# Optimization experiments

Hardware: AMD Instinct MI355X
Metric: run time of the kernel (lower is better)

The kernel has to match this reference:

```python
import jax, jax.numpy as jnp
import numpy as np

D, NH, DH, L, NCP, TW, NTP = 256, 8, 32, 4, 4, 2, 2
P = NCP + TW * NTP  # points per level per head
SHAPES = np.array([[4, 48, 64], [4, 24, 32], [4, 12, 16], [4, 6, 8]], dtype=np.int64)  # (T, H, W) per level


def _offset_biases():
    # Faithful to _reset_parameters: directional grid init for sampling-offset biases.
    thetas = np.arange(NH, dtype=np.float64) * (2.0 * np.pi / NH)
    grid = np.stack([np.cos(thetas), np.sin(thetas)], -1)
    grid = grid / np.abs(grid).max(-1, keepdims=True)
    curr = np.tile(grid.reshape(NH, 1, 1, 2), (1, L, NCP, 1))
    for i in range(NCP):
        curr[:, :, i, :] *= i + 1
    temp = np.tile(grid.reshape(NH, 1, 1, 1, 2), (1, L, TW, NTP, 1))
    init_offset = 0
    for pos, t in enumerate(range(1, TW + 1)):  # encoder default branch
        if t % 2:
            init_offset += 1
        for i in range(NTP):
            temp[:, :, pos, i, :] *= i + 1 + init_offset
    return curr.reshape(-1).astype(np.float32), temp.reshape(-1).astype(np.float32)


def setup_inputs() -> dict:
    key = jax.random.key(0)
    k = jax.random.split(key, 10)
    sizes = SHAPES[:, 0] * SHAPES[:, 1] * SHAPES[:, 2]
    Len_in = int(sizes.sum())  # 16320
    Lq, N = Len_in, 1
    b_so_np, b_tso_np = _offset_biases()
    return {
        "query": jax.random.normal(k[0], (N, Lq, D), jnp.float32),
        "reference_points": jax.random.uniform(k[1], (N, Lq, L, 2), jnp.float32),
        "temporal_offsets": jax.random.normal(k[2], (Lq, L, TW, 2), jnp.float32) * 0.02,
        "input_flatten": jax.random.normal(k[3], (N, Len_in, D), jnp.float32),
        "input_spatial_shapes": jnp.asarray(SHAPES),
        "input_level_start_index": jnp.asarray(np.concatenate([[0], np.cumsum(sizes)[:-1]]).astype(np.int64)),
        "W_so": jax.random.normal(k[4], (D, NH * L * NCP * 2), jnp.float32) * 0.01,
        "b_so": jnp.asarray(b_so_np),
        "W_tso": jax.random.normal(k[5], (D, NH * L * TW * NTP * 2), jnp.float32) * 0.01,
        "b_tso": jnp.asarray(b_tso_np),
        "W_aw": jax.random.normal(k[6], (D, NH * L * NCP), jnp.float32) * 0.02,
        "b_aw": jnp.zeros((NH * L * NCP,), jnp.float32),
        "W_taw": jax.random.normal(k[7], (D, NH * L * TW * NTP), jnp.float32) * 0.02,
        "b_taw": jnp.zeros((NH * L * TW * NTP,), jnp.float32),
        "W_v": jax.random.normal(k[8], (D, D), jnp.float32) / np.sqrt(D),
        "b_v": jnp.zeros((D,), jnp.float32),
        "W_o": jax.random.normal(k[9], (D, D), jnp.float32) / np.sqrt(D),
        "b_o": jnp.zeros((D,), jnp.float32),
    }


def _deform_core(value, loc, attn):
    # value: (N, Len_in, NH, DH); loc: (N, Lq, NH, L, P, 2) in [0,1]; attn: (N, Lq, NH, L, P)
    N, Lq = loc.shape[0], loc.shape[1]
    out = jnp.zeros((N, NH, Lq, DH), value.dtype)
    start = 0
    for l in range(L):  # small fixed level loop
        t, h, w = (int(s) for s in SHAPES[l])
        th = t * h  # frames stacked vertically -> grid is (T*H, W)
        npix = th * w
        v = value[:, start:start + npix].transpose(0, 2, 1, 3)  # (N, NH, npix, DH)
        # grid_sample semantics, align_corners=False, zero padding
        x = loc[:, :, :, l, :, 0] * w - 0.5
        y = loc[:, :, :, l, :, 1] * th - 0.5
        x0 = jnp.floor(x); y0 = jnp.floor(y)
        lx = x - x0; ly = y - y0
        x0i = x0.astype(jnp.int32); y0i = y0.astype(jnp.int32)

        def corner(xi, yi, wgt):
            inb = (xi >= 0) & (xi < w) & (yi >= 0) & (yi < th)
            idx = jnp.clip(yi, 0, th - 1) * w + jnp.clip(xi, 0, w - 1)  # (N,Lq,NH,P)
            idx = idx.transpose(0, 2, 1, 3).reshape(N, NH, Lq * P, 1)
            g = jnp.take_along_axis(v, idx, axis=2).reshape(N, NH, Lq, P, DH)
            wm = (wgt * inb).transpose(0, 2, 1, 3)  # (N,NH,Lq,P)
            return g * wm[..., None]

        samp = (corner(x0i, y0i, (1 - lx) * (1 - ly))
                + corner(x0i + 1, y0i, lx * (1 - ly))
                + corner(x0i, y0i + 1, (1 - lx) * ly)
                + corner(x0i + 1, y0i + 1, lx * ly))
        a = attn[:, :, :, l].transpose(0, 2, 1, 3)  # (N,NH,Lq,P)
        out = out + (samp * a[..., None]).sum(3)
        start += npix
    return out.transpose(0, 2, 1, 3).reshape(N, Lq, D)


def _forward(query, reference_points, temporal_offsets, input_flatten,
             W_so, b_so, W_tso, b_tso, W_aw, b_aw, W_taw, b_taw, W_v, b_v, W_o, b_o):
    N, Lq, _ = query.shape
    value = (input_flatten @ W_v + b_v).reshape(N, -1, NH, DH)
    cso = (query @ W_so + b_so).reshape(N, Lq, NH, L, NCP, 2)
    tso = (query @ W_tso + b_tso).reshape(N, Lq, NH, L, TW, NTP, 2)
    caw = (query @ W_aw + b_aw).reshape(N, Lq, NH, L * NCP)
    taw = (query @ W_taw + b_taw).reshape(N, Lq, NH, L * TW * NTP)
    aw = jax.nn.softmax(jnp.concatenate([caw, taw], -1), -1)  # joint softmax over curr+temporal
    attn = jnp.concatenate([aw[..., :L * NCP].reshape(N, Lq, NH, L, NCP),
                            aw[..., L * NCP:].reshape(N, Lq, NH, L, TW * NTP)], -1)
    # offset_normalizer = [W, T*H] per level
    norm = jnp.asarray(np.stack([SHAPES[:, 2], SHAPES[:, 0] * SHAPES[:, 1]], -1).astype(np.float32))
    tso_n = temporal_offsets[None, :, None, :, :, None, :] + tso / norm[None, None, None, :, None, None, :]
    tso_n = tso_n.reshape(N, Lq, NH, L, TW * NTP, 2)
    cso_n = cso / norm[None, None, None, :, None, :]
    loc = reference_points[:, :, None, :, None, :] + jnp.concatenate([cso_n, tso_n], 4)  # (N,Lq,NH,L,P,2)
    out = _deform_core(value, loc, attn)
    return out @ W_o + b_o


def reference(query, reference_points, temporal_offsets, input_flatten,
              input_spatial_shapes, input_level_start_index,
              W_so, b_so, W_tso, b_tso, W_aw, b_aw, W_taw, b_taw, W_v, b_v, W_o, b_o):
    return _forward(query, reference_points, temporal_offsets, input_flatten,
                    W_so, b_so, W_tso, b_tso, W_aw, b_aw, W_taw, b_taw, W_v, b_v, W_o, b_o)
```

## Files before the change

### kernel.cpp

```cpp
#include <hip/hip_runtime.h>


typedef unsigned short bfraw;
typedef __attribute__((ext_vector_type(2))) float f32x2;
typedef __attribute__((ext_vector_type(4))) float f32x4;
typedef __attribute__((ext_vector_type(8))) short bf16x8;

__device__ __forceinline__ float bf2f(bfraw u) {
  union { unsigned int i; float f; } v; v.i = ((unsigned int)u) << 16; return v.f;
}
__device__ __forceinline__ bfraw f2bf(float f) {
  union { float f; unsigned int i; } v; v.f = f;
  unsigned int x = v.i;
  return (bfraw)((x + 0x7FFFu + ((x >> 16) & 1u)) >> 16);
}
__device__ __forceinline__ float lo16f(unsigned int w) {
  union { unsigned int i; float f; } v; v.i = w << 16; return v.f;
}
__device__ __forceinline__ float hi16f(unsigned int w) {
  union { unsigned int i; float f; } v; v.i = w & 0xFFFF0000u; return v.f;
}
__device__ __forceinline__ float loadx(const void* p, size_t i, int f32m) {
  if (f32m) return ((const float*)p)[i];
  else      return bf2f(((const bfraw*)p)[i]);
}
__device__ __forceinline__ unsigned pk2(float a, float b) {
  return (unsigned)f2bf(a) | ((unsigned)f2bf(b) << 16);
}

__device__ __forceinline__ int vote_f32(const void* q) {
  const unsigned* p = (const unsigned*)q;
  int cnt = 0;
#pragma unroll
  for (int i = 0; i < 16; ++i) {
    const float a = fabsf(lo16f(p[i]));
    cnt += (a > 0.0009765625f && a < 16.0f) ? 1 : 0;
  }
  return (cnt >= 8) ? 0 : 1;
}

__device__ __forceinline__ void cvt8(const void* src, bfraw* dst, int i0, int f32m) {
  if (f32m) {
    const float4 a = ((const float4*)((const float*)src + i0))[0];
    const float4 b = ((const float4*)((const float*)src + i0))[1];
    uint4 o;
    o.x = pk2(a.x, a.y); o.y = pk2(a.z, a.w);
    o.z = pk2(b.x, b.y); o.w = pk2(b.z, b.w);
    *(uint4*)(dst + i0) = o;
  } else {
    *(uint4*)(dst + i0) = *(const uint4*)((const bfraw*)src + i0);
  }
}

__global__ __launch_bounds__(256) void prep_k(
    const void* W_v, const void* W_so, const void* W_tso,
    const void* W_aw, const void* W_taw, const void* W_o,
    const void* b_so, const void* b_tso, const void* b_aw, const void* b_taw,
    const void* b_v, const void* b_o,
    const void* refp, const void* toff,
    const void* query, const void* inflat,
    bfraw* __restrict__ WT, float* __restrict__ bcat,
    float* __restrict__ refpF, float* __restrict__ toffF,
    bfraw* __restrict__ queryB, bfraw* __restrict__ inflatB,
    int qbf, int ibf)
{
  const int f32m = vote_f32(query);
  const int b = blockIdx.x, t = threadIdx.x;
  if (b < 1280) {
    float s;
    if (b < 256)       s = loadx(W_v, (size_t)t * 256 + b, f32m);
    else if (b < 1024) {
      const int rp = b - 256;
      if (rp < 256)      s = loadx(W_so,  (size_t)t * 256 + rp, f32m);
      else if (rp < 512) s = loadx(W_tso, (size_t)t * 256 + (rp - 256), f32m);
      else if (rp < 640) s = loadx(W_aw,  (size_t)t * 128 + (rp - 512), f32m);
      else               s = loadx(W_taw, (size_t)t * 128 + (rp - 640), f32m);
    } else               s = loadx(W_o,  (size_t)t * 256 + (b - 1024), f32m);
    WT[(size_t)b * 256 + t] = f2bf(s);
  } else if (b < 1285) {
    const int i = (b - 1280) * 256 + t;
    if (i < 1280) {
      float s;
      if (i < 256)       s = loadx(b_so,  i, f32m);
      else if (i < 512)  s = loadx(b_tso, i - 256, f32m);
      else if (i < 640)  s = loadx(b_aw,  i - 512, f32m);
      else if (i < 768)  s = loadx(b_taw, i - 640, f32m);
      else if (i < 1024) s = loadx(b_v,   i - 768, f32m);
      else               s = loadx(b_o,   i - 1024, f32m);
      bcat[i] = s;
    }
  } else if (b < 1795) {
    const int i = (b - 1285) * 256 + t;
    refpF[i] = loadx(refp, i, f32m);
  } else if (b < 2815) {
    const int i = (b - 1795) * 256 + t;
    toffF[i] = loadx(toff, i, f32m);
  } else if (b < 4855) {
    if (!qbf) return;
    cvt8(query, queryB, (b - 2815) * 2048 + t * 8, f32m);
  } else {
    if (!ibf) return;
    cvt8(inflat, inflatB, (b - 4855) * 2048 + t * 8, f32m);
  }
}

__global__ __launch_bounds__(256) void gemmVP_k(
    const void* __restrict__ inflat, const void* __restrict__ query,
    const bfraw* __restrict__ inflatB, const bfraw* __restrict__ queryB,
    const bfraw* __restrict__ WT, const float* __restrict__ bcat,
    bfraw* __restrict__ valueOut, bfraw* __restrict__ proj, int M,
    int ibf, int qbf)
{
  __shared__ bfraw As[128][40];
  __shared__ bfraw Bs[128][40];
  const int y = blockIdx.y;
  const void* Araw; const bfraw* Abf; int wtb, colb, bmode, abf;
  if (y < 2) { Araw = inflat; Abf = inflatB; abf = ibf;
               wtb = y * 128;             colb = y * 128;       bmode = 1; }
  else       { Araw = query;  Abf = queryB;  abf = qbf;
               wtb = 256 + (y - 2) * 128; colb = (y - 2) * 128; bmode = 0; }
  const int f32m = abf ? 0 : vote_f32(query);

  const int bm = blockIdx.x * 128;
  const int tid = threadIdx.x;
  const int wave = tid >> 6, lane = tid & 63;
  const int quad = lane >> 4, l16 = lane & 15;
  const int mb = (wave >> 1) * 64, nb = (wave & 1) * 64;
  const int srow = tid >> 1;
  const int sk = (tid & 1) * 16;

  int lr = bm + srow; if (lr >= M) lr = M - 1;
  const size_t aoff = (size_t)lr * 256;

  f32x4 acc[4][4] = {{{0.f}}};

  for (int k0 = 0; k0 < 256; k0 += 32) {
    uint4 pa0, pa1;
    if (abf) {
      const bfraw* Ab = Abf + aoff + (k0 + sk);
      pa0 = ((const uint4*)Ab)[0];
      pa1 = ((const uint4*)Ab)[1];
    } else if (f32m) {
      const float* Af = (const float*)Araw + aoff + (k0 + sk);
      const float4 x0 = ((const float4*)Af)[0];
      const float4 x1 = ((const float4*)Af)[1];
      const float4 x2 = ((const float4*)Af)[2];
      const float4 x3 = ((const float4*)Af)[3];
      pa0.x = pk2(x0.x, x0.y); pa0.y = pk2(x0.z, x0.w);
      pa0.z = pk2(x1.x, x1.y); pa0.w = pk2(x1.z, x1.w);
      pa1.x = pk2(x2.x, x2.y); pa1.y = pk2(x2.z, x2.w);
      pa1.z = pk2(x3.x, x3.y); pa1.w = pk2(x3.z, x3.w);
    } else {
      const bfraw* Ab = (const bfraw*)Araw + aoff + (k0 + sk);
      pa0 = ((const uint4*)Ab)[0];
      pa1 = ((const uint4*)Ab)[1];
    }
    const bfraw* Bb = WT + (size_t)(wtb + srow) * 256 + (k0 + sk);
    const uint4 pb0 = ((const uint4*)Bb)[0];
    const uint4 pb1 = ((const uint4*)Bb)[1];
    *(uint4*)&As[srow][sk]     = pa0;
    *(uint4*)&As[srow][sk + 8] = pa1;
    *(uint4*)&Bs[srow][sk]     = pb0;
    *(uint4*)&Bs[srow][sk + 8] = pb1;
    __syncthreads();

    bf16x8 af[4], bf[4];
#pragma unroll
    for (int i = 0; i < 4; ++i)
      af[i] = *(const bf16x8*)&As[mb + i * 16 + l16][quad * 8];
#pragma unroll
    for (int j = 0; j < 4; ++j)
      bf[j] = *(const bf16x8*)&Bs[nb + j * 16 + l16][quad * 8];
#pragma unroll
    for (int i = 0; i < 4; ++i)
#pragma unroll
      for (int j = 0; j < 4; ++j)
        acc[i][j] = __builtin_amdgcn_mfma_f32_16x16x32_bf16(af[i], bf[j], acc[i][j], 0, 0, 0);
    __syncthreads();
  }

#pragma unroll
  for (int j = 0; j < 4; ++j) {
    const int col = colb + nb + j * 16 + l16;
    const float bb = bmode ? bcat[768 + col] : bcat[col];
#pragma unroll
    for (int i = 0; i < 4; ++i) {
#pragma unroll
      for (int r = 0; r < 4; ++r) {
        const int lrow = bm + mb + i * 16 + quad * 4 + r;
        if (lrow < M) {
          const float vv = acc[i][j][r] + bb;
          if (!bmode)
            proj[(size_t)lrow * 768 + col] = f2bf(vv);
          else
            valueOut[((unsigned)(col >> 5) * (unsigned)M + (unsigned)lrow) * 32u
                     + (unsigned)(col & 31)] = f2bf(vv);
        }
      }
    }
  }
}

__global__ __launch_bounds__(256) void gemmO_k(
    const bfraw* __restrict__ proj, const bfraw* __restrict__ WT,
    const float* __restrict__ bcat, void* __restrict__ Cout,
    const void* __restrict__ query, int M)
{
  __shared__ bfraw As[128][40];
  __shared__ bfraw Bs[128][40];
  const int f32m = vote_f32(query);
  const int bm = blockIdx.x * 128;
  const int bn = blockIdx.y * 128;
  const int tid = threadIdx.x;
  const int wave = tid >> 6, lane = tid & 63;
  const int quad = lane >> 4, l16 = lane & 15;
  const int mb = (wave >> 1) * 64, nb = (wave & 1) * 64;
  const int srow = tid >> 1;
  const int sk = (tid & 1) * 16;

  int lr = bm + srow; if (lr >= M) lr = M - 1;
  const size_t aoff = (size_t)lr * 768;

  f32x4 acc[4][4] = {{{0.f}}};

  for (int k0 = 0; k0 < 256; k0 += 32) {
    const bfraw* Ab = proj + aoff + (k0 + sk);
    const uint4 pa0 = ((const uint4*)Ab)[0];
    const uint4 pa1 = ((const uint4*)Ab)[1];
    const bfraw* Bb = WT + (size_t)(1024 + bn + srow) * 256 + (k0 + sk);
    const uint4 pb0 = ((const uint4*)Bb)[0];
    const uint4 pb1 = ((const uint4*)Bb)[1];
    *(uint4*)&As[srow][sk]     = pa0;
    *(uint4*)&As[srow][sk + 8] = pa1;
    *(uint4*)&Bs[srow][sk]     = pb0;
    *(uint4*)&Bs[srow][sk + 8] = pb1;
    __syncthreads();

    bf16x8 af[4], bf[4];
#pragma unroll
    for (int i = 0; i < 4; ++i)
      af[i] = *(const bf16x8*)&As[mb + i * 16 + l16][quad * 8];
#pragma unroll
    for (int j = 0; j < 4; ++j)
      bf[j] = *(const bf16x8*)&Bs[nb + j * 16 + l16][quad * 8];
#pragma unroll
    for (int i = 0; i < 4; ++i)
#pragma unroll
      for (int j = 0; j < 4; ++j)
        acc[i][j] = __builtin_amdgcn_mfma_f32_16x16x32_bf16(af[i], bf[j], acc[i][j], 0, 0, 0);
    __syncthreads();
  }

#pragma unroll
  for (int j = 0; j < 4; ++j) {
    const int col = bn + nb + j * 16 + l16;
    const float bb = bcat[1024 + col];
#pragma unroll
    for (int i = 0; i < 4; ++i) {
#pragma unroll
      for (int r = 0; r < 4; ++r) {
        const int lrow = bm + mb + i * 16 + quad * 4 + r;
        if (lrow < M) {
          const float v = acc[i][j][r] + bb;
          if (f32m) ((float*)Cout)[(size_t)lrow * 256 + col] = v;
          else      ((bfraw*)Cout)[(size_t)lrow * 256 + col] = f2bf(v);
        }
      }
    }
  }
}

__global__ __launch_bounds__(256) void sampler_k(
    bfraw* __restrict__ proj, const bfraw* __restrict__ value,
    const float* __restrict__ refp, const float* __restrict__ toff)
{
  __shared__ __align__(16) int   s_idx[256][4];
  __shared__ __align__(16) float s_w[256][4];

  const int h = blockIdx.y;
  const int tid = threadIdx.x;
  const int qi = tid >> 5;
  const int sp = tid & 31;
  const int l = sp >> 3;
  const int p = sp & 7;
  const int qg = blockIdx.x * 8 + qi;

  const int W_i[4]  = {64, 32, 16, 8};
  const int TH_i[4] = {192, 96, 48, 24};
  const int ST_i[4] = {0, 12288, 15360, 16128};
  const float Wf  = (float)W_i[l];
  const float THf = (float)TH_i[l];

  bfraw* prow = proj + (size_t)qg * 768;

  const float logit = (p < 4) ? bf2f(prow[512 + h * 16 + l * 4 + p])
                              : bf2f(prow[640 + h * 16 + l * 4 + (p - 4)]);
  float mx = logit;
#pragma unroll
  for (int m = 16; m >= 1; m >>= 1) mx = fmaxf(mx, __shfl_xor(mx, m));
  const float e = __expf(logit - mx);
  float ssum = e;
#pragma unroll
  for (int m = 16; m >= 1; m >>= 1) ssum += __shfl_xor(ssum, m);
  const float attn = e / ssum;

  const float rx = refp[(unsigned)(qg * 4 + l) * 2 + 0];
  const float ry = refp[(unsigned)(qg * 4 + l) * 2 + 1];
  float ox, oy;
  if (p < 4) {
    ox = bf2f(prow[h * 32 + l * 8 + p * 2 + 0]) / Wf;
    oy = bf2f(prow[h * 32 + l * 8 + p * 2 + 1]) / THf;
  } else {
    const int pj = p - 4, tw = pj >> 1, j = pj & 1;
    ox = toff[(unsigned)(qg * 4 + l) * 4 + tw * 2 + 0] +
         bf2f(prow[256 + h * 32 + l * 8 + tw * 4 + j * 2 + 0]) / Wf;
    oy = toff[(unsigned)(qg * 4 + l) * 4 + tw * 2 + 1] +
         bf2f(prow[256 + h * 32 + l * 8 + tw * 4 + j * 2 + 1]) / THf;
  }
  const float x = (rx + ox) * Wf - 0.5f;
  const float y = (ry + oy) * THf - 0.5f;
  const float x0f = floorf(x), y0f = floorf(y);
  const float lx = x - x0f, ly = y - y0f;
  const int x0 = (int)x0f, y0 = (int)y0f;
  const int Wg = W_i[l], THg = TH_i[l], ST = ST_i[l];
  const float cwx[2] = {1.f - lx, lx};
  const float cwy[2] = {1.f - ly, ly};
#pragma unroll
  for (int c = 0; c < 4; ++c) {
    const int xi = x0 + (c & 1), yi = y0 + (c >> 1);
    const bool inb = (xi >= 0) & (xi < Wg) & (yi >= 0) & (yi < THg);
    const int xc = min(max(xi, 0), Wg - 1);
    const int yc = min(max(yi, 0), THg - 1);
    s_idx[tid][c] = ST + yc * Wg + xc;
    s_w[tid][c] = inb ? (attn * cwx[c & 1] * cwy[c >> 1]) : 0.f;
  }
  __syncthreads();

  {
    const int pg = sp >> 2;
    const int chq = sp & 3;
    const char* vb = (const char*)(value + (unsigned)h * (16320u * 32u));
    const unsigned cb = (unsigned)(chq << 4);
    int   idx[16];
    float ww[16];
#pragma unroll
    for (int pt = 0; pt < 4; ++pt) {
      const int ds = qi * 32 + pg * 4 + pt;
      const int4   ia = *(const int4*)&s_idx[ds][0];
      const float4 wa = *(const float4*)&s_w[ds][0];
      idx[pt * 4 + 0] = ia.x; idx[pt * 4 + 1] = ia.y;
      idx[pt * 4 + 2] = ia.z; idx[pt * 4 + 3] = ia.w;
      ww[pt * 4 + 0] = wa.x; ww[pt * 4 + 1] = wa.y;
      ww[pt * 4 + 2] = wa.z; ww[pt * 4 + 3] = wa.w;
    }
#define GLD(n) const uint4 v##n = *(const uint4*)(vb + ((((unsigned)idx[n]) << 6) | cb))
    GLD(0); GLD(1); GLD(2); GLD(3); GLD(4); GLD(5); GLD(6); GLD(7);
    GLD(8); GLD(9); GLD(10); GLD(11); GLD(12); GLD(13); GLD(14); GLD(15);
#undef GLD
    f32x2 a0 = {0.f, 0.f}, a1 = {0.f, 0.f}, a2 = {0.f, 0.f}, a3 = {0.f, 0.f};
#define CONS(n) {                                            \
    const float w = ww[n];                                   \
    const f32x2 w2 = {w, w};                                 \
    f32x2 t;                                                 \
    t.x = lo16f(v##n.x); t.y = hi16f(v##n.x); a0 += w2 * t;  \
    t.x = lo16f(v##n.y); t.y = hi16f(v##n.y); a1 += w2 * t;  \
    t.x = lo16f(v##n.z); t.y = hi16f(v##n.z); a2 += w2 * t;  \
    t.x = lo16f(v##n.w); t.y = hi16f(v##n.w); a3 += w2 * t;  }
    CONS(0); CONS(1); CONS(2); CONS(3); CONS(4); CONS(5); CONS(6); CONS(7);
    CONS(8); CONS(9); CONS(10); CONS(11); CONS(12); CONS(13); CONS(14); CONS(15);
#undef CONS
    float acc[8] = {a0.x, a0.y, a1.x, a1.y, a2.x, a2.y, a3.x, a3.y};
#pragma unroll
    for (int m = 4; m <= 16; m <<= 1)
#pragma unroll
      for (int r = 0; r < 8; ++r)
        acc[r] += __shfl_xor(acc[r], m);
    if (pg == 0) {
      uint4 pk;
      pk.x = pk2(acc[0], acc[1]);
      pk.y = pk2(acc[2], acc[3]);
      pk.z = pk2(acc[4], acc[5]);
      pk.w = pk2(acc[6], acc[7]);
      *(uint4*)(prow + h * 32 + chq * 8) = pk;
    }
  }
}

extern "C" void kernel_launch(void* const* d_in, const int* in_sizes, int n_in,
                              void* d_out, int out_size, void* d_ws, size_t ws_size,
                              hipStream_t stream)
{
  const void* query  = d_in[0];
  const void* refp   = d_in[1];
  const void* toff   = d_in[2];
  const void* inflat = d_in[3];
  const void* W_so  = d_in[6];
  const void* b_so  = d_in[7];
  const void* W_tso = d_in[8];
  const void* b_tso = d_in[9];
  const void* W_aw  = d_in[10];
  const void* b_aw  = d_in[11];
  const void* W_taw = d_in[12];
  const void* b_taw = d_in[13];
  const void* W_v   = d_in[14];
  const void* b_v   = d_in[15];
  const void* W_o   = d_in[16];
  const void* b_o   = d_in[17];

  const int Lq = 16320;
  const size_t WT_B   = (size_t)1280 * 256 * 2;
  const size_t BCAT_B = 1280 * 4;
  const size_t REFP_B = (size_t)Lq * 8 * 4;
  const size_t TOFF_B = (size_t)Lq * 16 * 4;
  const size_t VAL_B  = (size_t)8 * Lq * 32 * 2;
  const size_t PROJ_B = (size_t)Lq * 768 * 2;
  const size_t QB_B   = (size_t)Lq * 256 * 2;
  const size_t base   = WT_B + BCAT_B + REFP_B + TOFF_B + VAL_B + PROJ_B;

  const int qbf = (ws_size >= base + QB_B)     ? 1 : 0;
  const int ibf = (ws_size >= base + 2 * QB_B) ? 1 : 0;

  char* wp = (char*)d_ws;
  bfraw* WT     = (bfraw*)wp; wp += WT_B;
  float* bcat   = (float*)wp; wp += BCAT_B;
  float* refpF  = (float*)wp; wp += REFP_B;
  float* toffF  = (float*)wp; wp += TOFF_B;
  bfraw* value  = (bfraw*)wp; wp += VAL_B;
  bfraw* proj   = (bfraw*)wp; wp += PROJ_B;
  bfraw* queryB = (bfraw*)wp; wp += QB_B;
  bfraw* inflatB= (bfraw*)wp;

  const dim3 blk(256);
  const int prep_blocks = ibf ? 6895 : (qbf ? 4855 : 2815);
  prep_k<<<dim3(prep_blocks), blk, 0, stream>>>(
      W_v, W_so, W_tso, W_aw, W_taw, W_o,
      b_so, b_tso, b_aw, b_taw, b_v, b_o,
      refp, toff, query, inflat,
      WT, bcat, refpF, toffF, queryB, inflatB, qbf, ibf);
  gemmVP_k<<<dim3(128, 8), blk, 0, stream>>>(inflat, query, inflatB, queryB,
                                             WT, bcat, value, proj, Lq, ibf, qbf);
  sampler_k<<<dim3(Lq / 8, 8), blk, 0, stream>>>(proj, value, refpF, toffF);
  gemmO_k<<<dim3(128, 2), blk, 0, stream>>>(proj, WT, bcat, d_out, query, Lq);
}
```

Before: 221.6 us.

## Drop LDS staging in GEMMs and load MFMA fragments directly from global

```diff
diff --git a/kernel.cpp b/kernel.cpp
--- a/kernel.cpp
+++ b/kernel.cpp
@@ -111,8 +111,6 @@
     bfraw* __restrict__ valueOut, bfraw* __restrict__ proj, int M,
     int ibf, int qbf)
 {
-  __shared__ bfraw As[128][40];
-  __shared__ bfraw Bs[128][40];
   const int y = blockIdx.y;
   const void* Araw; const bfraw* Abf; int wtb, colb, bmode, abf;
   if (y < 2) { Araw = inflat; Abf = inflatB; abf = ibf;
@@ -126,59 +124,53 @@
   const int wave = tid >> 6, lane = tid & 63;
   const int quad = lane >> 4, l16 = lane & 15;
   const int mb = (wave >> 1) * 64, nb = (wave & 1) * 64;
-  const int srow = tid >> 1;
-  const int sk = (tid & 1) * 16;
-
-  int lr = bm + srow; if (lr >= M) lr = M - 1;
-  const size_t aoff = (size_t)lr * 256;
+
+  size_t aoff[4]; const bfraw* bptr[4];
+#pragma unroll
+  for (int i = 0; i < 4; ++i) {
+    int row = bm + mb + i * 16 + l16; if (row >= M) row = M - 1;
+    aoff[i] = (size_t)row * 256 + quad * 8;
+  }
+#pragma unroll
+  for (int j = 0; j < 4; ++j)
+    bptr[j] = WT + (size_t)(wtb + nb + j * 16 + l16) * 256 + quad * 8;
 
   f32x4 acc[4][4] = {{{0.f}}};
 
+#pragma unroll
   for (int k0 = 0; k0 < 256; k0 += 32) {
-    uint4 pa0, pa1;
+    bf16x8 af[4], bf[4];
     if (abf) {
-      const bfraw* Ab = Abf + aoff + (k0 + sk);
-      pa0 = ((const uint4*)Ab)[0];
-      pa1 = ((const uint4*)Ab)[1];
+#pragma unroll
+      for (int i = 0; i < 4; ++i)
+        af[i] = *(const bf16x8*)(Abf + aoff[i] + k0);
     } else if (f32m) {
-      const float* Af = (const float*)Araw + aoff + (k0 + sk);
-      const float4 x0 = ((const float4*)Af)[0];
-      const float4 x1 = ((const float4*)Af)[1];
-      const float4 x2 = ((const float4*)Af)[2];
-      const float4 x3 = ((const float4*)Af)[3];
-      pa0.x = pk2(x0.x, x0.y); pa0.y = pk2(x0.z, x0.w);
-      pa0.z = pk2(x1.x, x1.y); pa0.w = pk2(x1.z, x1.w);
-      pa1.x = pk2(x2.x, x2.y); pa1.y = pk2(x2.z, x2.w);
-      pa1.z = pk2(x3.x, x3.y); pa1.w = pk2(x3.z, x3.w);
+#pragma unroll
+      for (int i = 0; i < 4; ++i) {
+        const float* Af = (const float*)Araw + aoff[i] + k0;
+        const float4 x0 = ((const float4*)Af)[0];
+        const float4 x1 = ((const float4*)Af)[1];
+        uint4 o;
+        o.x = pk2(x0.x, x0.y); o.y = pk2(x0.z, x0.w);
+        o.z = pk2(x1.x, x1.y); o.w = pk2(x1.z, x1.w);
+        af[i] = *(const bf16x8*)&o;
+      }
     } else {
-      const bfraw* Ab = (const bfraw*)Araw + aoff + (k0 + sk);
-      pa0 = ((const uint4*)Ab)[0];
-      pa1 = ((const uint4*)Ab)[1];
-    }
-    const bfraw* Bb = WT + (size_t)(wtb + srow) * 256 + (k0 + sk);
-    const uint4 pb0 = ((const uint4*)Bb)[0];
-    const uint4 pb1 = ((const uint4*)Bb)[1];
-    *(uint4*)&As[srow][sk]     = pa0;
-    *(uint4*)&As[srow][sk + 8] = pa1;
-    *(uint4*)&Bs[srow][sk]     = pb0;
-    *(uint4*)&Bs[srow][sk + 8] = pb1;
-    __syncthreads();
-
-    bf16x8 af[4], bf[4];
-#pragma unroll
-    for (int i = 0; i < 4; ++i)
-      af[i] = *(const bf16x8*)&As[mb + i * 16 + l16][quad * 8];
+#pragma unroll
+      for (int i = 0; i < 4; ++i)
+        af[i] = *(const bf16x8*)((const bfraw*)Araw + aoff[i] + k0);
+    }
 #pragma unroll
     for (int j = 0; j < 4; ++j)
-      bf[j] = *(const bf16x8*)&Bs[nb + j * 16 + l16][quad * 8];
+      bf[j] = *(const bf16x8*)(bptr[j] + k0);
 #pragma unroll
     for (int i = 0; i < 4; ++i)
 #pragma unroll
       for (int j = 0; j < 4; ++j)
         acc[i][j] = __builtin_amdgcn_mfma_f32_16x16x32_bf16(af[i], bf[j], acc[i][j], 0, 0, 0);
-    __syncthreads();
-  }
-
+  }
+
+  const int quad4 = quad * 4;
 #pragma unroll
   for (int j = 0; j < 4; ++j) {
     const int col = colb + nb + j * 16 + l16;
@@ -187,7 +179,7 @@
     for (int i = 0; i < 4; ++i) {
 #pragma unroll
       for (int r = 0; r < 4; ++r) {
-        const int lrow = bm + mb + i * 16 + quad * 4 + r;
+        const int lrow = bm + mb + i * 16 + quad4 + r;
         if (lrow < M) {
           const float vv = acc[i][j][r] + bb;
           if (!bmode)
@@ -206,8 +198,6 @@
     const float* __restrict__ bcat, void* __restrict__ Cout,
     const void* __restrict__ query, int M)
 {
-  __shared__ bfraw As[128][40];
-  __shared__ bfraw Bs[128][40];
   const int f32m = vote_f32(query);
   const int bm = blockIdx.x * 128;
   const int bn = blockIdx.y * 128;
@@ -215,42 +205,36 @@
   const int wave = tid >> 6, lane = tid & 63;
   const int quad = lane >> 4, l16 = lane & 15;
   const int mb = (wave >> 1) * 64, nb = (wave & 1) * 64;
-  const int srow = tid >> 1;
-  const int sk = (tid & 1) * 16;
-
-  int lr = bm + srow; if (lr >= M) lr = M - 1;
-  const size_t aoff = (size_t)lr * 768;
+
+  const bfraw* aptr[4]; const bfraw* bptr[4];
+#pragma unroll
+  for (int i = 0; i < 4; ++i) {
+    int row = bm + mb + i * 16 + l16; if (row >= M) row = M - 1;
+    aptr[i] = proj + (size_t)row * 768 + quad * 8;
+  }
+#pragma unroll
+  for (int j = 0; j < 4; ++j)
+    bptr[j] = WT + (size_t)(1024 + bn + nb + j * 16 + l16) * 256 + quad * 8;
 
   f32x4 acc[4][4] = {{{0.f}}};
 
+#pragma unroll
   for (int k0 = 0; k0 < 256; k0 += 32) {
-    const bfraw* Ab = proj + aoff + (k0 + sk);
-    const uint4 pa0 = ((const uint4*)Ab)[0];
-    const uint4 pa1 = ((const uint4*)Ab)[1];
-    const bfraw* Bb = WT + (size_t)(1024 + bn + srow) * 256 + (k0 + sk);
-    const uint4 pb0 = ((const uint4*)Bb)[0];
-    const uint4 pb1 = ((const uint4*)Bb)[1];
-    *(uint4*)&As[srow][sk]     = pa0;
-    *(uint4*)&As[srow][sk + 8] = pa1;
-    *(uint4*)&Bs[srow][sk]     = pb0;
-    *(uint4*)&Bs[srow][sk + 8] = pb1;
-    __syncthreads();
-
     bf16x8 af[4], bf[4];
 #pragma unroll
     for (int i = 0; i < 4; ++i)
-      af[i] = *(const bf16x8*)&As[mb + i * 16 + l16][quad * 8];
+      af[i] = *(const bf16x8*)(aptr[i] + k0);
 #pragma unroll
     for (int j = 0; j < 4; ++j)
-      bf[j] = *(const bf16x8*)&Bs[nb + j * 16 + l16][quad * 8];
+      bf[j] = *(const bf16x8*)(bptr[j] + k0);
 #pragma unroll
     for (int i = 0; i < 4; ++i)
 #pragma unroll
       for (int j = 0; j < 4; ++j)
         acc[i][j] = __builtin_amdgcn_mfma_f32_16x16x32_bf16(af[i], bf[j], acc[i][j], 0, 0, 0);
-    __syncthreads();
-  }
-
+  }
+
+  const int quad4 = quad * 4;
 #pragma unroll
   for (int j = 0; j < 4; ++j) {
     const int col = bn + nb + j * 16 + l16;
@@ -259,7 +243,7 @@
     for (int i = 0; i < 4; ++i) {
 #pragma unroll
       for (int r = 0; r < 4; ++r) {
-        const int lrow = bm + mb + i * 16 + quad * 4 + r;
+        const int lrow = bm + mb + i * 16 + quad4 + r;
         if (lrow < M) {
           const float v = acc[i][j][r] + bb;
           if (f32m) ((float*)Cout)[(size_t)lrow * 256 + col] = v;
@@ -285,11 +269,15 @@
   const int p = sp & 7;
   const int qg = blockIdx.x * 8 + qi;
 
-  const int W_i[4]  = {64, 32, 16, 8};
-  const int TH_i[4] = {192, 96, 48, 24};
-  const int ST_i[4] = {0, 12288, 15360, 16128};
-  const float Wf  = (float)W_i[l];
-  const float THf = (float)TH_i[l];
+  const int Wg  = 64 >> l;
+  const int THg = 192 >> l;
+  const int ST  = 16384 - (16384 >> (2 * l));
+  const int sh  = 6 - l;
+  const float Wf  = (float)Wg;
+  const float THf = (float)THg;
+  union { unsigned u; float f; } rwu; rwu.u = 0x3C800000u + ((unsigned)l << 23);
+  const float rW  = rwu.f;
+  const float rTH = rW * 0.33333333333333333f;
 
   bfraw* prow = proj + (size_t)qg * 768;
 
@@ -302,36 +290,35 @@
   float ssum = e;
 #pragma unroll
   for (int m = 16; m >= 1; m >>= 1) ssum += __shfl_xor(ssum, m);
-  const float attn = e / ssum;
+  const float attn = e * __builtin_amdgcn_rcpf(ssum);
 
   const float rx = refp[(unsigned)(qg * 4 + l) * 2 + 0];
   const float ry = refp[(unsigned)(qg * 4 + l) * 2 + 1];
   float ox, oy;
   if (p < 4) {
-    ox = bf2f(prow[h * 32 + l * 8 + p * 2 + 0]) / Wf;
-    oy = bf2f(prow[h * 32 + l * 8 + p * 2 + 1]) / THf;
+    ox = bf2f(prow[h * 32 + l * 8 + p * 2 + 0]) * rW;
+    oy = bf2f(prow[h * 32 + l * 8 + p * 2 + 1]) * rTH;
   } else {
     const int pj = p - 4, tw = pj >> 1, j = pj & 1;
     ox = toff[(unsigned)(qg * 4 + l) * 4 + tw * 2 + 0] +
-         bf2f(prow[256 + h * 32 + l * 8 + tw * 4 + j * 2 + 0]) / Wf;
+         bf2f(prow[256 + h * 32 + l * 8 + tw * 4 + j * 2 + 0]) * rW;
     oy = toff[(unsigned)(qg * 4 + l) * 4 + tw * 2 + 1] +
-         bf2f(prow[256 + h * 32 + l * 8 + tw * 4 + j * 2 + 1]) / THf;
+         bf2f(prow[256 + h * 32 + l * 8 + tw * 4 + j * 2 + 1]) * rTH;
   }
   const float x = (rx + ox) * Wf - 0.5f;
   const float y = (ry + oy) * THf - 0.5f;
   const float x0f = floorf(x), y0f = floorf(y);
   const float lx = x - x0f, ly = y - y0f;
   const int x0 = (int)x0f, y0 = (int)y0f;
-  const int Wg = W_i[l], THg = TH_i[l], ST = ST_i[l];
   const float cwx[2] = {1.f - lx, lx};
   const float cwy[2] = {1.f - ly, ly};
 #pragma unroll
   for (int c = 0; c < 4; ++c) {
     const int xi = x0 + (c & 1), yi = y0 + (c >> 1);
-    const bool inb = (xi >= 0) & (xi < Wg) & (yi >= 0) & (yi < THg);
+    const bool inb = ((unsigned)xi < (unsigned)Wg) & ((unsigned)yi < (unsigned)THg);
     const int xc = min(max(xi, 0), Wg - 1);
     const int yc = min(max(yi, 0), THg - 1);
-    s_idx[tid][c] = ST + yc * Wg + xc;
+    s_idx[tid][c] = ST + (yc << sh) + xc;
     s_w[tid][c] = inb ? (attn * cwx[c & 1] * cwy[c >> 1]) : 0.f;
   }
   __syncthreads();
```

Measured after the change: 237.7 us. +7.3%, slower.
